# Optimization experiments

Measured on AMD Instinct MI355X. Metric: run time of the kernel, lower is better.

The kernel has to match this reference:

```python
import jax, jax.numpy as jnp
import numpy as np


def setup_inputs() -> dict:
    key = jax.random.key(0)
    k1, k2 = jax.random.split(key)
    B, H, W, C = 128, 28, 28, 128
    x = jax.random.normal(k1, (B, H, W, C), dtype=jnp.float32)
    # template bank: [C, H, W, H, W] -- indexed by (channel, argmax_row, argmax_col)
    t_p = jax.random.uniform(k2, (C, H, W, H, W), dtype=jnp.float32)
    return {"x": x, "t_p": t_p}


def reference(x, t_p):
    B, H, W, C = x.shape
    # global spatial argmax per (batch, channel) == max_pool_with_argmax with ksize=(H,W)
    flat_idx = jnp.argmax(x.reshape(B, H * W, C), axis=1)  # [B, C]
    h = flat_idx // W  # [B, C]
    w = flat_idx % W   # [B, C]
    c_idx = jnp.arange(C)[None, :]  # [1, C] broadcast against [B, C]
    # gather per-(b,c) template: t_p[c, h*, w*, :, :] -> [B, C, H, W]
    templates = t_p[c_idx, h, w]  # [B, C, H, W]
    templates = jnp.transpose(templates, (0, 2, 3, 1))  # [B, H, W, C]
    masked = jax.nn.relu(x * templates)
    return (masked, x, templates)
```

## Files before the change

### kernel.cpp

```cpp
#include <hip/hip_runtime.h>


constexpr int HWc = 784, Cc = 128, Bc = 128;

typedef float f4 __attribute__((ext_vector_type(4)));
typedef int i4 __attribute__((ext_vector_type(4)));

__device__ inline void nt_store(float* p, f4 v) {
  __builtin_nontemporal_store(v, (f4*)p);
}

__global__ __launch_bounds__(512) void argmax_copy_kernel(
    const float* __restrict__ x, float* __restrict__ ox,
    float* __restrict__ pmax, int* __restrict__ pidx) {
  int chunk = blockIdx.x;
  int b = blockIdx.y;
  int t = threadIdx.x;
  int c4 = t & 31;
  int part = t >> 5;
  int ch = c4 << 2;

  int cbase = chunk * 392;
  int s0 = cbase + part * 25;
  int send = s0 + 25;
  if (send > cbase + 392) send = cbase + 392;

  const size_t plane = (size_t)HWc * Cc;
  const float* xp = x + (size_t)b * plane + ch;
  float* oxp = ox + (size_t)b * plane + ch;

  f4 best = {-3.4e38f, -3.4e38f, -3.4e38f, -3.4e38f};
  i4 bi = {s0, s0, s0, s0};
  for (int s = s0; s < send; ++s) {
    f4 v = *(const f4*)(xp + (size_t)s * Cc);
    nt_store(oxp + (size_t)s * Cc, v);
    if (v[0] > best[0]) { best[0] = v[0]; bi[0] = s; }
    if (v[1] > best[1]) { best[1] = v[1]; bi[1] = s; }
    if (v[2] > best[2]) { best[2] = v[2]; bi[2] = s; }
    if (v[3] > best[3]) { best[3] = v[3]; bi[3] = s; }
  }

  __shared__ float smax[16][Cc];
  __shared__ int sidx[16][Cc];
  *(f4*)&smax[part][ch] = best;
  *(i4*)&sidx[part][ch] = bi;
  __syncthreads();

  if (t < Cc) {
    float m = smax[0][t];
    int mi = sidx[0][t];
#pragma unroll
    for (int p = 1; p < 16; ++p) {
      float v = smax[p][t];
      if (v > m) { m = v; mi = sidx[p][t]; }
    }
    int o = (b * 2 + chunk) * Cc + t;
    pmax[o] = m;
    pidx[o] = mi;
  }
}

__global__ __launch_bounds__(256) void out_kernel(
    const float* __restrict__ x, const float* __restrict__ tp,
    const float* __restrict__ pmax, const int* __restrict__ pidx,
    float* __restrict__ out) {
  int b = blockIdx.y;
  int t = threadIdx.x;

  __shared__ int tbase[Cc];
  if (t < Cc) {
    int base = b * 2 * Cc + t;
    float m = pmax[base];
    int mi = pidx[base];
    float v = pmax[base + Cc];
    if (v > m) { m = v; mi = pidx[base + Cc]; }
    tbase[t] = (t * HWc + mi) * HWc;
  }
  __syncthreads();

  int c4 = t & 31;
  int u = t >> 5;
  int ch = c4 << 2;

  const float* r0 = tp + tbase[ch + 0];
  const float* r1 = tp + tbase[ch + 1];
  const float* r2 = tp + tbase[ch + 2];
  const float* r3 = tp + tbase[ch + 3];

  const size_t plane = (size_t)HWc * Cc;
  size_t bplane = (size_t)b * plane;
  float* om = out;
  float* ot = out + 2 * (size_t)Bc * plane;
  int sb = blockIdx.x * 56;

#pragma unroll
  for (int k = 0; k < 2; ++k) {
    int idx = u + (k << 3);
    if (idx < 14) {
      int s0 = sb + (idx << 2);
      size_t off = bplane + (size_t)s0 * Cc + ch;
      const float* xp = x + off;

      f4 xv0 = *(const f4*)(xp);
      f4 xv1 = *(const f4*)(xp + Cc);
      f4 xv2 = *(const f4*)(xp + 2 * Cc);
      f4 xv3 = *(const f4*)(xp + 3 * Cc);
      f4 tv0 = *(const f4*)(r0 + s0);
      f4 tv1 = *(const f4*)(r1 + s0);
      f4 tv2 = *(const f4*)(r2 + s0);
      f4 tv3 = *(const f4*)(r3 + s0);

      float* omp = om + off;
      float* otp = ot + off;

#pragma unroll
      for (int i = 0; i < 4; ++i) {
        f4 xvi = (i == 0) ? xv0 : (i == 1) ? xv1 : (i == 2) ? xv2 : xv3;
        f4 tcol = {tv0[i], tv1[i], tv2[i], tv3[i]};
        f4 mv;
        mv[0] = fmaxf(xvi[0] * tcol[0], 0.f);
        mv[1] = fmaxf(xvi[1] * tcol[1], 0.f);
        mv[2] = fmaxf(xvi[2] * tcol[2], 0.f);
        mv[3] = fmaxf(xvi[3] * tcol[3], 0.f);
        nt_store(omp + i * Cc, mv);
        nt_store(otp + i * Cc, tcol);
      }
    }
  }
}

extern "C" void kernel_launch(void* const* d_in, const int* in_sizes, int n_in,
                              void* d_out, int out_size, void* d_ws,
                              size_t ws_size, hipStream_t stream) {
  const float* x = (const float*)d_in[0];
  const float* tp = (const float*)d_in[1];
  float* out = (float*)d_out;
  float* ox = out + (size_t)Bc * HWc * Cc;

  float* pmax = (float*)d_ws;
  int* pidx = (int*)((char*)d_ws + (size_t)Bc * 2 * Cc * sizeof(float));

  argmax_copy_kernel<<<dim3(2, Bc), 512, 0, stream>>>(x, ox, pmax, pidx);
  out_kernel<<<dim3(14, Bc), 256, 0, stream>>>(x, tp, pmax, pidx, out);
}
```

Baseline: 56.95 us.

## Stage gathered template rows through shared-memory transpose and double grid parallelism

The argmax/copy kernel is split into four spatial chunks per batch instead of two, giving more blocks. The output kernel first loads each channel's template row segment with coalesced 16-byte nontemporal loads into a padded shared-memory tile, then reads it back transposed for the channel-innermost outputs. This replaces scattered per-thread strided gathers from four template rows. It adds an extra shared-memory pass and barrier, and each block now handles 28 spatial positions with only 7 of 8 warps active in the compute phase.

```diff
diff --git a/kernel.cpp b/kernel.cpp
--- a/kernel.cpp
+++ b/kernel.cpp
@@ -2,12 +2,18 @@
 
 
 constexpr int HWc = 784, Cc = 128, Bc = 128;
+constexpr int K1S = 196;
+constexpr int K2S = 28;
+constexpr int LDW = 132;
 
 typedef float f4 __attribute__((ext_vector_type(4)));
 typedef int i4 __attribute__((ext_vector_type(4)));
 
 __device__ inline void nt_store(float* p, f4 v) {
   __builtin_nontemporal_store(v, (f4*)p);
+}
+__device__ inline f4 nt_load4(const float* p) {
+  return __builtin_nontemporal_load((const f4*)p);
 }
 
 __global__ __launch_bounds__(512) void argmax_copy_kernel(
@@ -16,14 +22,12 @@
   int chunk = blockIdx.x;
   int b = blockIdx.y;
   int t = threadIdx.x;
-  int c4 = t & 31;
-  int part = t >> 5;
-  int ch = c4 << 2;
+  int c4 = t & 31, part = t >> 5, ch = c4 << 2;
 
-  int cbase = chunk * 392;
-  int s0 = cbase + part * 25;
-  int send = s0 + 25;
-  if (send > cbase + 392) send = cbase + 392;
+  int cbase = chunk * K1S;
+  int s0 = cbase + part * 13;
+  int send = s0 + 13;
+  if (send > cbase + K1S) send = cbase + K1S;
 
   const size_t plane = (size_t)HWc * Cc;
   const float* xp = x + (size_t)b * plane + ch;
@@ -54,7 +58,7 @@
       float v = smax[p][t];
       if (v > m) { m = v; mi = sidx[p][t]; }
     }
-    int o = (b * 2 + chunk) * Cc + t;
+    int o = (b * 4 + chunk) * Cc + t;
     pmax[o] = m;
     pidx[o] = mi;
   }
@@ -64,67 +68,82 @@
     const float* __restrict__ x, const float* __restrict__ tp,
     const float* __restrict__ pmax, const int* __restrict__ pidx,
     float* __restrict__ out) {
+  int sx = blockIdx.x;
   int b = blockIdx.y;
   int t = threadIdx.x;
+  int sb = sx * K2S;
 
   __shared__ int tbase[Cc];
+  __shared__ float tl[K2S * LDW];
+
   if (t < Cc) {
-    int base = b * 2 * Cc + t;
+    int base = b * 4 * Cc + t;
     float m = pmax[base];
     int mi = pidx[base];
-    float v = pmax[base + Cc];
-    if (v > m) { m = v; mi = pidx[base + Cc]; }
+#pragma unroll
+    for (int p = 1; p < 4; ++p) {
+      float v = pmax[base + p * Cc];
+      if (v > m) { m = v; mi = pidx[base + p * Cc]; }
+    }
     tbase[t] = (t * HWc + mi) * HWc;
   }
   __syncthreads();
 
-  int c4 = t & 31;
-  int u = t >> 5;
-  int ch = c4 << 2;
+  {
+    int c0 = t >> 2, q = t & 3;
+#pragma unroll
+    for (int batch = 0; batch < 2; ++batch) {
+      int c = c0 + (batch << 6);
+      const float* row = tp + tbase[c] + sb;
+#pragma unroll
+      for (int j = 0; j < 2; ++j) {
+        int s4 = q + (j << 2);
+        if (s4 < 7) {
+          f4 v = nt_load4(row + (s4 << 2));
+          int sl = s4 << 2;
+          tl[(sl + 0) * LDW + c] = v[0];
+          tl[(sl + 1) * LDW + c] = v[1];
+          tl[(sl + 2) * LDW + c] = v[2];
+          tl[(sl + 3) * LDW + c] = v[3];
+        }
+      }
+    }
+  }
+  __syncthreads();
 
-  const float* r0 = tp + tbase[ch + 0];
-  const float* r1 = tp + tbase[ch + 1];
-  const float* r2 = tp + tbase[ch + 2];
-  const float* r3 = tp + tbase[ch + 3];
+  int c4 = t & 31, u = t >> 5, ch = c4 << 2;
+  if (u < 7) {
+    const size_t plane = (size_t)HWc * Cc;
+    size_t bplane = (size_t)b * plane;
+    int s0 = sb + (u << 2);
+    size_t off = bplane + (size_t)s0 * Cc + ch;
+    const float* xp = x + off;
 
-  const size_t plane = (size_t)HWc * Cc;
-  size_t bplane = (size_t)b * plane;
-  float* om = out;
-  float* ot = out + 2 * (size_t)Bc * plane;
-  int sb = blockIdx.x * 56;
+    f4 xv0 = *(const f4*)(xp);
+    f4 xv1 = *(const f4*)(xp + Cc);
+    f4 xv2 = *(const f4*)(xp + 2 * Cc);
+    f4 xv3 = *(const f4*)(xp + 3 * Cc);
+
+    int sl = u << 2;
+    f4 tc0 = *(const f4*)&tl[(sl + 0) * LDW + ch];
+    f4 tc1 = *(const f4*)&tl[(sl + 1) * LDW + ch];
+    f4 tc2 = *(const f4*)&tl[(sl + 2) * LDW + ch];
+    f4 tc3 = *(const f4*)&tl[(sl + 3) * LDW + ch];
+
+    float* omp = out + off;
+    float* otp = out + 2 * (size_t)Bc * plane + off;
 
 #pragma unroll
-  for (int k = 0; k < 2; ++k) {
-    int idx = u + (k << 3);
-    if (idx < 14) {
-      int s0 = sb + (idx << 2);
-      size_t off = bplane + (size_t)s0 * Cc + ch;
-      const float* xp = x + off;
-
-      f4 xv0 = *(const f4*)(xp);
-      f4 xv1 = *(const f4*)(xp + Cc);
-      f4 xv2 = *(const f4*)(xp + 2 * Cc);
-      f4 xv3 = *(const f4*)(xp + 3 * Cc);
-      f4 tv0 = *(const f4*)(r0 + s0);
-      f4 tv1 = *(const f4*)(r1 + s0);
-      f4 tv2 = *(const f4*)(r2 + s0);
-      f4 tv3 = *(const f4*)(r3 + s0);
-
-      float* omp = om + off;
-      float* otp = ot + off;
-
-#pragma unroll
-      for (int i = 0; i < 4; ++i) {
-        f4 xvi = (i == 0) ? xv0 : (i == 1) ? xv1 : (i == 2) ? xv2 : xv3;
-        f4 tcol = {tv0[i], tv1[i], tv2[i], tv3[i]};
-        f4 mv;
-        mv[0] = fmaxf(xvi[0] * tcol[0], 0.f);
-        mv[1] = fmaxf(xvi[1] * tcol[1], 0.f);
-        mv[2] = fmaxf(xvi[2] * tcol[2], 0.f);
-        mv[3] = fmaxf(xvi[3] * tcol[3], 0.f);
-        nt_store(omp + i * Cc, mv);
-        nt_store(otp + i * Cc, tcol);
-      }
+    for (int i = 0; i < 4; ++i) {
+      f4 xvi = (i == 0) ? xv0 : (i == 1) ? xv1 : (i == 2) ? xv2 : xv3;
+      f4 tc = (i == 0) ? tc0 : (i == 1) ? tc1 : (i == 2) ? tc2 : tc3;
+      f4 mv;
+      mv[0] = fmaxf(xvi[0] * tc[0], 0.f);
+      mv[1] = fmaxf(xvi[1] * tc[1], 0.f);
+      mv[2] = fmaxf(xvi[2] * tc[2], 0.f);
+      mv[3] = fmaxf(xvi[3] * tc[3], 0.f);
+      nt_store(omp + i * Cc, mv);
+      nt_store(otp + i * Cc, tc);
     }
   }
 }
@@ -138,8 +157,8 @@
   float* ox = out + (size_t)Bc * HWc * Cc;
 
   float* pmax = (float*)d_ws;
-  int* pidx = (int*)((char*)d_ws + (size_t)Bc * 2 * Cc * sizeof(float));
+  int* pidx = (int*)((char*)d_ws + (size_t)Bc * 4 * Cc * sizeof(float));
 
-  argmax_copy_kernel<<<dim3(2, Bc), 512, 0, stream>>>(x, ox, pmax, pidx);
-  out_kernel<<<dim3(14, Bc), 256, 0, stream>>>(x, tp, pmax, pidx, out);
+  argmax_copy_kernel<<<dim3(4, Bc), 512, 0, stream>>>(x, ox, pmax, pidx);
+  out_kernel<<<dim3(28, Bc), 256, 0, stream>>>(x, tp, pmax, pidx, out);
 }
```

Measured after the change: 72.42 us. 27.2% more time.
